# Kernel optimization log

Measured on AMD Instinct MI355X. Metric: run time of the kernel, lower is better.

## Reference

```python
import jax, jax.numpy as jnp
import numpy as np

B, P, T, V, N, D = 16, 96, 128, 64, 16, 128


def setup_inputs() -> dict:
    key = jax.random.key(0)
    ks = jax.random.split(key, 9)
    s = 0.05  # weight scale for stability
    return {
        "queries": jax.random.normal(ks[0], (B, P, V, D), jnp.float32),
        "keys": jax.random.normal(ks[1], (B, T, V, D), jnp.float32),
        "var_ccc": jax.random.randint(ks[2], (B, V, N), 0, V),
        "Wq": jax.random.normal(ks[3], (D, D), jnp.float32) * s,
        "bq": jnp.zeros((D,), jnp.float32),
        "Wkv": jax.random.normal(ks[4], (D, D), jnp.float32) * s,
        "bkv": jnp.zeros((D,), jnp.float32),
        "Wout": jax.random.normal(ks[5], (D, D), jnp.float32) * s,
        "bout": jnp.zeros((D,), jnp.float32),
    }


def reference(queries, keys, var_ccc, Wq, bq, Wkv, bkv, Wout, bout):
    b, p, v, d = queries.shape
    scale = d ** -0.5
    # projections (nn.Linear: x @ W.T + b)
    q = queries @ Wq.T + bq                      # [B,P,V,D]
    k = keys @ Wkv.T + bkv                       # [B,T,V,D]
    k_last = k[:, -p:]                           # [B,P,V,D]
    # irregular gather of neighbor keys per (batch, variable)
    idx = var_ccc.reshape(b, -1)                 # [B, V*N]
    kc = jax.vmap(lambda kb, ib: kb[:, ib])(k_last, idx)  # [B,P,V*N,D]
    kc = kc.reshape(b, p, v, -1, d)              # [B,P,V,N,D] (keys == values)
    # tiny 1xN attention per (b,p,v)
    scores = jnp.einsum('bpvd,bpvnd->bpvn', q, kc) * scale
    attn = jax.nn.softmax(scores, axis=-1)       # dropout is identity in eval
    out = jnp.einsum('bpvn,bpvnd->bpvd', attn, kc)  # [B,P,V,D]
    res = jnp.concatenate([k[:, :-p], out], axis=1)  # [B,T,V,D]
    return res @ Wout.T + bout
```

## Files before the change

### kernel.cpp

```cpp
#include <hip/hip_runtime.h>

#define BB 16
#define PP 96
#define TT 128
#define VV 64
#define NN 16
#define DD 128
#define BPP (BB * PP)
#define NPASS (BB * 32)
#define SB 136
#define ST 72
#define SSF 68
#define SCALE 0.08838834764831845f
#define SLICE 4352

typedef __bf16 bf16x8 __attribute__((ext_vector_type(8)));
typedef __bf16 bf16x4 __attribute__((ext_vector_type(4)));
typedef float  floatx4 __attribute__((ext_vector_type(4)));
typedef unsigned int uint32x4 __attribute__((ext_vector_type(4)));

#define MFMA16(a, b, c) __builtin_amdgcn_mfma_f32_16x16x32_bf16(a, b, c, 0, 0, 0)

__device__ __forceinline__ bf16x8 cvt8(float4 a, float4 b) {
    return bf16x8{(__bf16)a.x, (__bf16)a.y, (__bf16)a.z, (__bf16)a.w,
                  (__bf16)b.x, (__bf16)b.y, (__bf16)b.z, (__bf16)b.w};
}

__device__ __forceinline__ void loadA_g(const float* Xs, int lm, int lq, bf16x8 af[4]) {
    const float4* p = (const float4*)(Xs + lm * DD + lq * 8);
#pragma unroll
    for (int ks = 0; ks < 4; ++ks) af[ks] = cvt8(p[8 * ks], p[8 * ks + 1]);
}

__device__ __forceinline__ void loadA_l(const __bf16* As, int sa, int lm, int lq,
                                        bf16x8* af, int kblocks) {
#pragma unroll
    for (int ks = 0; ks < 4; ++ks) {
        if (ks >= kblocks) break;
        af[ks] = *(const bf16x8*)(As + lm * sa + lq * 8 + 32 * ks);
    }
}

__device__ __forceinline__ void mmB(const bf16x8* af, const __bf16* B, int sb,
                                    int lm, int lq, floatx4* acc, int nblocks, int kblocks) {
#pragma unroll
    for (int nb = 0; nb < 8; ++nb) {
        if (nb >= nblocks) break;
        acc[nb] = floatx4{0.f, 0.f, 0.f, 0.f};
#pragma unroll
        for (int ks = 0; ks < 4; ++ks) {
            if (ks >= kblocks) break;
            bf16x8 bf = *(const bf16x8*)(B + (nb * 16 + lm) * sb + lq * 8 + 32 * ks);
            acc[nb] = MFMA16(af[ks], bf, acc[nb]);
        }
    }
}

__global__ void prep(const float* __restrict__ Wq, const float* __restrict__ Wkv,
                     const float* __restrict__ Wout, const float* __restrict__ bkv,
                     const float* __restrict__ bout,
                     __bf16* __restrict__ Wb, float* __restrict__ bcomb) {
    int i = blockIdx.x, j = threadIdx.x;
    Wb[i * DD + j]         = (__bf16)Wq[i * DD + j];
    Wb[16384 + i * DD + j] = (__bf16)Wkv[i * DD + j];
    Wb[32768 + i * DD + j] = (__bf16)Wout[i * DD + j];
    float acc = 0.f;
    for (int k = 0; k < DD; ++k) acc += Wout[i * DD + k] * Wkv[k * DD + j];
    Wb[49152 + i * DD + j] = (__bf16)acc;
    if (i == 0) {
        float bs = bout[j];
        for (int k = 0; k < DD; ++k) bs += Wout[j * DD + k] * bkv[k];
        bcomb[j] = bs;
    }
}

__global__ __launch_bounds__(256, 3) void fused(
    const float* __restrict__ queries, const float* __restrict__ keys,
    const int* __restrict__ ccc, const __bf16* __restrict__ Wb,
    const float* __restrict__ bq, const float* __restrict__ bkv,
    const float* __restrict__ bout, const float* __restrict__ bcomb,
    float* __restrict__ out) {
    __shared__ __align__(16) char lds[53248];
    __bf16* R1    = (__bf16*)lds;
    __bf16* smKs  = (__bf16*)(lds + 17408);
    __bf16* smKsT = (__bf16*)(lds + 34816);
    float*  smS   = (float*)lds;

    int bl = blockIdx.x, t = threadIdx.x;
    int w = t >> 6, L = t & 63, lm = L & 15, lq = L >> 4;

    bf16x8 af[4];
    floatx4 acc[8];

    if (bl >= BPP) {
        int pb = bl - BPP;
        int b = pb >> 5, wi = pb & 31;
        const float* Xs = keys + ((long)b * TT * VV + wi * 64 + w * 16) * DD;
        float* Yg = out + ((long)b * TT * VV + wi * 64) * DD;
        loadA_g(Xs, lm, lq, af);
        mmB(af, Wb + 49152, DD, lm, lq, acc, 8, 4);
#pragma unroll
        for (int nb = 0; nb < 8; ++nb) {
            float bv = bcomb[nb * 16 + lm];
#pragma unroll
            for (int r = 0; r < 4; ++r)
                Yg[(long)(w * 16 + lq * 4 + r) * DD + nb * 16 + lm] = acc[nb][r] + bv;
        }
        return;
    }

    int b = bl / PP, p = bl % PP;
    const float* Qg = queries + ((long)(b * PP + p) * VV) * DD;
    const float* Kg = keys + ((long)(b * TT + 32 + p) * VV) * DD;
    float* Yg = out + ((long)(b * TT + 32 + p) * VV) * DD;

    float4 kr[8];
    {
        const float4* kp = (const float4*)(Kg + (w * 16 + lm) * DD + lq * 8);
#pragma unroll
        for (int ks = 0; ks < 4; ++ks) {
            kr[2 * ks] = kp[8 * ks]; kr[2 * ks + 1] = kp[8 * ks + 1];
        }
    }

#pragma unroll
    for (int ks = 0; ks < 4; ++ks) af[ks] = cvt8(kr[2 * ks], kr[2 * ks + 1]);
    mmB(af, Wb + 16384, DD, lm, lq, acc, 8, 4);

    float4 qr[8];
    {
        const float4* qp = (const float4*)(Qg + (w * 16 + lm) * DD + lq * 8);
#pragma unroll
        for (int ks = 0; ks < 4; ++ks) {
            qr[2 * ks] = qp[8 * ks]; qr[2 * ks + 1] = qp[8 * ks + 1];
        }
    }

#pragma unroll
    for (int nb = 0; nb < 8; ++nb) {
        float bv = bkv[nb * 16 + lm];
        bf16x4 tp;
#pragma unroll
        for (int r = 0; r < 4; ++r) {
            float vv = acc[nb][r] + bv;
            smKs[(w * 16 + lq * 4 + r) * SB + nb * 16 + lm] = (__bf16)vv;
            tp[r] = (__bf16)vv;
        }
        *(bf16x4*)(smKsT + (nb * 16 + lm) * ST + w * 16 + lq * 4) = tp;
    }

    int se[NN];
    {
        const int4* cp = (const int4*)(ccc + ((long)b * VV + w * 16 + lm) * NN);
#pragma unroll
        for (int i = 0; i < 4; ++i) {
            int4 c4 = cp[i];
            se[4 * i] = c4.x; se[4 * i + 1] = c4.y;
            se[4 * i + 2] = c4.z; se[4 * i + 3] = c4.w;
        }
    }
    __syncthreads();

#pragma unroll
    for (int ks = 0; ks < 4; ++ks) af[ks] = cvt8(qr[2 * ks], qr[2 * ks + 1]);
    mmB(af, Wb, DD, lm, lq, acc, 8, 4);
#pragma unroll
    for (int nb = 0; nb < 8; ++nb) {
        float bv = bq[nb * 16 + lm];
#pragma unroll
        for (int r = 0; r < 4; ++r)
            R1[(w * 16 + lq * 4 + r) * SB + nb * 16 + lm] = (__bf16)(acc[nb][r] + bv);
    }

    loadA_l(R1 + w * 16 * SB, SB, lm, lq, af, 4);
    mmB(af, smKs, SB, lm, lq, acc, 4, 4);
#pragma unroll
    for (int nb = 0; nb < 4; ++nb)
#pragma unroll
        for (int r = 0; r < 4; ++r)
            smS[(w * 16 + lq * 4 + r) * SSF + nb * 16 + lm] = acc[nb][r];

    __bf16* smAsl = (__bf16*)(lds + w * SLICE);
    {
        int g = lq;
        float sg[NN];
        const float* Srow = smS + (w * 16 + lm) * SSF;
#pragma unroll
        for (int n = 0; n < NN; ++n) sg[n] = Srow[se[n]];
        __builtin_amdgcn_sched_barrier(0);
        {
            uint32x4 z{0u, 0u, 0u, 0u};
            char* zb = (char*)smAsl + (L >> 2) * (ST * 2) + (L & 3) * 32;
            *(uint32x4*)zb = z;
            *(uint32x4*)(zb + 16) = z;
        }
        float mx = -1e30f;
#pragma unroll
        for (int n = 0; n < NN; ++n) { sg[n] *= SCALE; mx = fmaxf(mx, sg[n]); }
        float sum = 0.f;
#pragma unroll
        for (int n = 0; n < NN; ++n) { sg[n] = __expf(sg[n] - mx); sum += sg[n]; }
        float inv = 1.f / sum;
#pragma unroll
        for (int j = 0; j < 4; ++j) {
            int u = se[g * 4 + j];
            float tot = 0.f;
#pragma unroll
            for (int n = 0; n < NN; ++n) tot += (se[n] == u) ? sg[n] : 0.f;
            smAsl[lm * ST + u] = (__bf16)(tot * inv);
        }
    }

    loadA_l(smAsl, ST, lm, lq, af, 2);
    mmB(af, smKsT, ST, lm, lq, acc, 8, 2);
#pragma unroll
    for (int nb = 0; nb < 8; ++nb)
#pragma unroll
        for (int r = 0; r < 4; ++r)
            R1[(w * 16 + lq * 4 + r) * SB + nb * 16 + lm] = (__bf16)acc[nb][r];

    loadA_l(R1 + w * 16 * SB, SB, lm, lq, af, 4);
    mmB(af, Wb + 32768, DD, lm, lq, acc, 8, 4);
#pragma unroll
    for (int nb = 0; nb < 8; ++nb) {
        float bv = bout[nb * 16 + lm];
#pragma unroll
        for (int r = 0; r < 4; ++r)
            Yg[(long)(w * 16 + lq * 4 + r) * DD + nb * 16 + lm] = acc[nb][r] + bv;
    }
}

extern "C" void kernel_launch(void* const* d_in, const int* in_sizes, int n_in,
                              void* d_out, int out_size, void* d_ws, size_t ws_size,
                              hipStream_t stream) {
    const float* queries = (const float*)d_in[0];
    const float* keys    = (const float*)d_in[1];
    const int*   ccc     = (const int*)d_in[2];
    const float* Wq      = (const float*)d_in[3];
    const float* bq      = (const float*)d_in[4];
    const float* Wkv     = (const float*)d_in[5];
    const float* bkv     = (const float*)d_in[6];
    const float* Wout    = (const float*)d_in[7];
    const float* bout    = (const float*)d_in[8];
    float* out = (float*)d_out;

    __bf16* Wb    = (__bf16*)d_ws;
    float*  bcomb = (float*)((char*)d_ws + 131072);

    prep<<<dim3(128), dim3(128), 0, stream>>>(Wq, Wkv, Wout, bkv, bout, Wb, bcomb);

    fused<<<dim3(BPP + NPASS), dim3(256), 0, stream>>>(
        queries, keys, ccc, Wb, bq, bkv, bout, bcomb, out);
}
```

Measured before the change: 232.5 us.

## Fold key projection into query and output weights to drop per-block GEMMs

Precomputes Wq^T·Wkv so the query is projected straight into raw-key space and scores use the raw keys, and precomputes Wout·Wkv so the attention output multiplies raw keys and goes straight to the output projection. The attention path in each block now runs two 128x128 projections instead of four, with no intermediate out-of-attention round trip through shared memory. The cost is a slightly heavier prep kernel and some change in bf16 rounding, since the folded weights are rounded once rather than rounding the intermediates.

```diff
diff --git a/kernel.cpp b/kernel.cpp
--- a/kernel.cpp
+++ b/kernel.cpp
@@ -57,33 +57,38 @@
 }
 
 __global__ void prep(const float* __restrict__ Wq, const float* __restrict__ Wkv,
-                     const float* __restrict__ Wout, const float* __restrict__ bkv,
-                     const float* __restrict__ bout,
-                     __bf16* __restrict__ Wb, float* __restrict__ bcomb) {
+                     const float* __restrict__ Wout, const float* __restrict__ bq,
+                     const float* __restrict__ bkv, const float* __restrict__ bout,
+                     __bf16* __restrict__ Wb, float* __restrict__ bcomb,
+                     float* __restrict__ bqk) {
     int i = blockIdx.x, j = threadIdx.x;
-    Wb[i * DD + j]         = (__bf16)Wq[i * DD + j];
-    Wb[16384 + i * DD + j] = (__bf16)Wkv[i * DD + j];
-    Wb[32768 + i * DD + j] = (__bf16)Wout[i * DD + j];
-    float acc = 0.f;
-    for (int k = 0; k < DD; ++k) acc += Wout[i * DD + k] * Wkv[k * DD + j];
-    Wb[49152 + i * DD + j] = (__bf16)acc;
+    float m1 = 0.f, wc = 0.f;
+    for (int k = 0; k < DD; ++k) {
+        m1 += Wq[k * DD + j] * Wkv[k * DD + i];
+        wc += Wout[i * DD + k] * Wkv[k * DD + j];
+    }
+    Wb[i * DD + j]         = (__bf16)m1;
+    Wb[16384 + i * DD + j] = (__bf16)wc;
     if (i == 0) {
-        float bs = bout[j];
-        for (int k = 0; k < DD; ++k) bs += Wout[j * DD + k] * bkv[k];
+        float bs = bout[j], bk = 0.f;
+        for (int k = 0; k < DD; ++k) {
+            bs += Wout[j * DD + k] * bkv[k];
+            bk += bq[k] * Wkv[k * DD + j];
+        }
         bcomb[j] = bs;
+        bqk[j] = bk;
     }
 }
 
 __global__ __launch_bounds__(256, 3) void fused(
     const float* __restrict__ queries, const float* __restrict__ keys,
     const int* __restrict__ ccc, const __bf16* __restrict__ Wb,
-    const float* __restrict__ bq, const float* __restrict__ bkv,
-    const float* __restrict__ bout, const float* __restrict__ bcomb,
+    const float* __restrict__ bqk, const float* __restrict__ bcomb,
     float* __restrict__ out) {
     __shared__ __align__(16) char lds[53248];
     __bf16* R1    = (__bf16*)lds;
-    __bf16* smKs  = (__bf16*)(lds + 17408);
-    __bf16* smKsT = (__bf16*)(lds + 34816);
+    __bf16* smK   = (__bf16*)(lds + 17408);
+    __bf16* smKCT = (__bf16*)(lds + 34816);
     float*  smS   = (float*)lds;
 
     int bl = blockIdx.x, t = threadIdx.x;
@@ -98,7 +103,7 @@
         const float* Xs = keys + ((long)b * TT * VV + wi * 64 + w * 16) * DD;
         float* Yg = out + ((long)b * TT * VV + wi * 64) * DD;
         loadA_g(Xs, lm, lq, af);
-        mmB(af, Wb + 49152, DD, lm, lq, acc, 8, 4);
+        mmB(af, Wb + 16384, DD, lm, lq, acc, 8, 4);
 #pragma unroll
         for (int nb = 0; nb < 8; ++nb) {
             float bv = bcomb[nb * 16 + lm];
@@ -137,16 +142,26 @@
     }
 
 #pragma unroll
-    for (int nb = 0; nb < 8; ++nb) {
-        float bv = bkv[nb * 16 + lm];
+    for (int ks = 0; ks < 4; ++ks)
+        *(bf16x8*)(smK + (w * 16 + lm) * SB + lq * 8 + 32 * ks) = af[ks];
+
+#pragma unroll
+    for (int nb = 0; nb < 8; ++nb) {
         bf16x4 tp;
 #pragma unroll
-        for (int r = 0; r < 4; ++r) {
-            float vv = acc[nb][r] + bv;
-            smKs[(w * 16 + lq * 4 + r) * SB + nb * 16 + lm] = (__bf16)vv;
-            tp[r] = (__bf16)vv;
-        }
-        *(bf16x4*)(smKsT + (nb * 16 + lm) * ST + w * 16 + lq * 4) = tp;
+        for (int r = 0; r < 4; ++r) tp[r] = (__bf16)acc[nb][r];
+        *(bf16x4*)(smKCT + (nb * 16 + lm) * ST + w * 16 + lq * 4) = tp;
+    }
+
+#pragma unroll
+    for (int ks = 0; ks < 4; ++ks) af[ks] = cvt8(qr[2 * ks], qr[2 * ks + 1]);
+    mmB(af, Wb, DD, lm, lq, acc, 8, 4);
+#pragma unroll
+    for (int nb = 0; nb < 8; ++nb) {
+        float bv = bqk[nb * 16 + lm];
+#pragma unroll
+        for (int r = 0; r < 4; ++r)
+            R1[(w * 16 + lq * 4 + r) * SB + nb * 16 + lm] = (__bf16)(acc[nb][r] + bv);
     }
 
     int se[NN];
@@ -161,19 +176,8 @@
     }
     __syncthreads();
 
-#pragma unroll
-    for (int ks = 0; ks < 4; ++ks) af[ks] = cvt8(qr[2 * ks], qr[2 * ks + 1]);
-    mmB(af, Wb, DD, lm, lq, acc, 8, 4);
-#pragma unroll
-    for (int nb = 0; nb < 8; ++nb) {
-        float bv = bq[nb * 16 + lm];
-#pragma unroll
-        for (int r = 0; r < 4; ++r)
-            R1[(w * 16 + lq * 4 + r) * SB + nb * 16 + lm] = (__bf16)(acc[nb][r] + bv);
-    }
-
     loadA_l(R1 + w * 16 * SB, SB, lm, lq, af, 4);
-    mmB(af, smKs, SB, lm, lq, acc, 4, 4);
+    mmB(af, smK, SB, lm, lq, acc, 4, 4);
 #pragma unroll
     for (int nb = 0; nb < 4; ++nb)
 #pragma unroll
@@ -212,18 +216,10 @@
     }
 
     loadA_l(smAsl, ST, lm, lq, af, 2);
-    mmB(af, smKsT, ST, lm, lq, acc, 8, 2);
-#pragma unroll
-    for (int nb = 0; nb < 8; ++nb)
-#pragma unroll
-        for (int r = 0; r < 4; ++r)
-            R1[(w * 16 + lq * 4 + r) * SB + nb * 16 + lm] = (__bf16)acc[nb][r];
-
-    loadA_l(R1 + w * 16 * SB, SB, lm, lq, af, 4);
-    mmB(af, Wb + 32768, DD, lm, lq, acc, 8, 4);
-#pragma unroll
-    for (int nb = 0; nb < 8; ++nb) {
-        float bv = bout[nb * 16 + lm];
+    mmB(af, smKCT, ST, lm, lq, acc, 8, 2);
+#pragma unroll
+    for (int nb = 0; nb < 8; ++nb) {
+        float bv = bcomb[nb * 16 + lm];
 #pragma unroll
         for (int r = 0; r < 4; ++r)
             Yg[(long)(w * 16 + lq * 4 + r) * DD + nb * 16 + lm] = acc[nb][r] + bv;
@@ -245,10 +241,11 @@
     float* out = (float*)d_out;
 
     __bf16* Wb    = (__bf16*)d_ws;
-    float*  bcomb = (float*)((char*)d_ws + 131072);
-
-    prep<<<dim3(128), dim3(128), 0, stream>>>(Wq, Wkv, Wout, bkv, bout, Wb, bcomb);
+    float*  bcomb = (float*)((char*)d_ws + 65536);
+    float*  bqk   = (float*)((char*)d_ws + 66048);
+
+    prep<<<dim3(128), dim3(128), 0, stream>>>(Wq, Wkv, Wout, bq, bkv, bout, Wb, bcomb, bqk);
 
     fused<<<dim3(BPP + NPASS), dim3(256), 0, stream>>>(
-        queries, keys, ccc, Wb, bq, bkv, bout, bcomb, out);
-}
+        queries, keys, ccc, Wb, bqk, bcomb, out);
+}
```

Measured after the change: 225.6 us. 3.0% less time.
